# Optimization experiments

Hardware: AMD Instinct MI355X
Metric: run time of the kernel (lower is better)

Reference implementation:

```python
import jax, jax.numpy as jnp
import numpy as np

DIM = 1024
HEADS = 16
HEAD_DIM = DIM // HEADS
WINDOW = 128


def setup_inputs() -> dict:
    key = jax.random.key(0)
    k1, k2, k3, k4 = jax.random.split(key, 4)
    B, T = 2, 2048
    x = jax.random.normal(k1, (B, T, DIM), dtype=jnp.float32)
    # nn.Linear(dim, 3*dim, bias=False): weight [3*dim, dim]; y = x @ W.T
    W_qkv = jax.random.normal(k2, (3 * DIM, DIM), dtype=jnp.float32) * (1.0 / np.sqrt(DIM))
    W_proj = jax.random.normal(k3, (DIM, DIM), dtype=jnp.float32) * (1.0 / np.sqrt(DIM))
    b_proj = jax.random.normal(k4, (DIM,), dtype=jnp.float32) * 0.01
    return {"x": x, "W_qkv": W_qkv, "W_proj": W_proj, "b_proj": b_proj}


def reference(x, W_qkv, W_proj, b_proj) -> jnp.ndarray:
    B, T, C = x.shape
    scale = HEAD_DIM ** -0.5
    qkv = jnp.einsum('btc,oc->bto', x, W_qkv)  # [B,T,3*D]
    qkv = qkv.reshape(B, T, 3, HEADS, HEAD_DIM)
    qkv = jnp.transpose(qkv, (2, 0, 3, 1, 4))  # [3,B,H,T,hd]
    q, k, v = qkv[0], qkv[1], qkv[2]
    # sliding-window mask: attend iff |i-j| <= WINDOW
    idx = jnp.arange(T)
    mask = jnp.abs(idx[:, None] - idx[None, :]) <= WINDOW  # [T,T]
    scores = jnp.einsum('bhqd,bhkd->bhqk', q, k) * scale  # [B,H,T,T]
    scores = jnp.where(mask[None, None], scores, jnp.finfo(scores.dtype).min)
    attn = jax.nn.softmax(scores, axis=-1)
    out = jnp.einsum('bhqk,bhkd->bhqd', attn, v)  # [B,H,T,hd]
    out = jnp.transpose(out, (0, 2, 1, 3)).reshape(B, T, C)
    return jnp.einsum('btc,oc->bto', out, W_proj) + b_proj
```

## Files before the change

kernel.cpp:

```cpp
#include <hip/hip_runtime.h>
#include <hip/hip_bf16.h>
#include <cstdint>
#include <cstddef>

#define DIMC 1024
#define HEADS 16
#define HD 64
#define WINDOW 128
#define BB 2
#define TT 2048
#define NTOK (BB*TT)
#define QKVN (3*DIMC)

typedef __bf16 bf16;
typedef __bf16 bf16x8 __attribute__((ext_vector_type(8)));
typedef __bf16 bf16x4 __attribute__((ext_vector_type(4)));
typedef float f32x4 __attribute__((ext_vector_type(4)));
typedef unsigned int u32;

typedef const __attribute__((address_space(1))) u32* gp1_t;
typedef __attribute__((address_space(3))) u32* lp3_t;

__device__ __forceinline__ void gload16(const void* g, void* l) {
  __builtin_amdgcn_global_load_lds((gp1_t)g, (lp3_t)l, 16, 0, 0);
}

__device__ __forceinline__ u32 lds_u32(const void* p) {
  return (u32)(uintptr_t)(__attribute__((address_space(3))) const void*)p;
}

__device__ __forceinline__ void BAR() {
  asm volatile("" ::: "memory");
  __builtin_amdgcn_s_barrier();
  asm volatile("" ::: "memory");
}

__global__ void cast3_kernel(const float* __restrict__ x,
                             const float* __restrict__ wq,
                             const float* __restrict__ wp,
                             bf16* __restrict__ xo,
                             bf16* __restrict__ wqo,
                             bf16* __restrict__ wpo) {
  const int NX = NTOK * DIMC / 4;
  const int NQ = QKVN * DIMC / 4;
  const int NP = DIMC * DIMC / 4;
  const int total = NX + NQ + NP;
  typedef float float4v __attribute__((ext_vector_type(4)));
  for (int i = blockIdx.x * blockDim.x + threadIdx.x; i < total;
       i += gridDim.x * blockDim.x) {
    const float4v* src; bf16* dst; int j;
    if (i < NX)            { src = (const float4v*)x;  dst = xo;  j = i; }
    else if (i < NX + NQ)  { src = (const float4v*)wq; dst = wqo; j = i - NX; }
    else                   { src = (const float4v*)wp; dst = wpo; j = i - NX - NQ; }
    float4v v = src[j];
    bf16x4 o;
    o[0] = (bf16)v[0]; o[1] = (bf16)v[1]; o[2] = (bf16)v[2]; o[3] = (bf16)v[3];
    ((bf16x4*)dst)[j] = o;
  }
}

__device__ __forceinline__ bf16x8 lds_frag(const bf16* base, int row, int colb) {
  const char* p = (const char*)base + row * 128 + (colb ^ ((row & 7) << 4));
  return *(const bf16x8*)p;
}

template<int BN, int N_, bool BF16OUT>
__global__ __launch_bounds__(256, 2) void gemm_kernel(
    const bf16* __restrict__ A, const bf16* __restrict__ Bw,
    bf16* __restrict__ Cb, float* __restrict__ Cf,
    const float* __restrict__ bias) {
  constexpr int NT = 16;
  constexpr int NB = BN / 32;
  constexpr int LPT = 4 + BN / 32;
  __shared__ bf16 Al[2][128 * 64];
  __shared__ bf16 Bl[2][BN * 64];

  const int tid = threadIdx.x;
  const int w = tid >> 6, l = tid & 63;
  const int wm = w >> 1, wn = w & 1;
  const int lr = l & 15, lg = l >> 4;

  const int nwg = gridDim.x;
  const int bid = blockIdx.x;
  const int wg = (bid & 7) * (nwg >> 3) + (bid >> 3);
  const int bm = wg & 31;
  const int bn = wg >> 5;

  const char* Ag = (const char*)A + (size_t)(bm * 128) * 2048;
  const char* Bg = (const char*)Bw + (size_t)(bn * BN) * 2048;

  auto stageA = [&](bf16* lds, int kt) {
#pragma unroll
    for (int i = 0; i < 4; i++) {
      const int R0 = w * 32 + i * 8;
      const int r = R0 + (l >> 3);
      const char* src = Ag + (size_t)r * 2048 + kt * 128
                        + (((l & 7) * 16) ^ ((r & 7) << 4));
      gload16(src, lds + R0 * 64);
    }
  };
  auto stageB = [&](bf16* lds, int kt) {
#pragma unroll
    for (int i = 0; i < NB; i++) {
      const int R0 = w * (BN / 4) + i * 8;
      const int r = R0 + (l >> 3);
      const char* src = Bg + (size_t)r * 2048 + kt * 128
                        + (((l & 7) * 16) ^ ((r & 7) << 4));
      gload16(src, lds + R0 * 64);
    }
  };

  stageA(Al[0], 0); stageB(Bl[0], 0);
  stageA(Al[1], 1); stageB(Bl[1], 1);
  if constexpr (LPT == 7) asm volatile("s_waitcnt vmcnt(7)" ::: "memory");
  else                    asm volatile("s_waitcnt vmcnt(8)" ::: "memory");
  BAR();

  f32x4 acc[4][NB] = {};

  for (int kt = 0; kt < NT; ++kt) {
    const bf16* Ac = Al[kt & 1];
    const bf16* Bc = Bl[kt & 1];

    bf16x8 af[4][2], bf[NB][2];
#pragma unroll
    for (int m = 0; m < 4; m++)
#pragma unroll
      for (int kk = 0; kk < 2; kk++)
        af[m][kk] = lds_frag(Ac, wm * 64 + m * 16 + lr, kk * 64 + lg * 16);
#pragma unroll
    for (int n = 0; n < NB; n++)
#pragma unroll
      for (int kk = 0; kk < 2; kk++)
        bf[n][kk] = lds_frag(Bc, wn * (BN / 2) + n * 16 + lr, kk * 64 + lg * 16);

    asm volatile("s_waitcnt lgkmcnt(0)" ::: "memory");
    __builtin_amdgcn_sched_barrier(0);
    BAR();

    if (kt + 2 < NT) {
      stageA(Al[kt & 1], kt + 2);
      stageB(Bl[kt & 1], kt + 2);
    }

    __builtin_amdgcn_s_setprio(1);
#pragma unroll
    for (int kk = 0; kk < 2; kk++)
#pragma unroll
      for (int m = 0; m < 4; m++)
#pragma unroll
        for (int n = 0; n < NB; n++)
          acc[m][n] = __builtin_amdgcn_mfma_f32_16x16x32_bf16(
              af[m][kk], bf[n][kk], acc[m][n], 0, 0, 0);
    __builtin_amdgcn_s_setprio(0);

    if (kt < NT - 2) {
      if constexpr (LPT == 7) asm volatile("s_waitcnt vmcnt(7)" ::: "memory");
      else                    asm volatile("s_waitcnt vmcnt(8)" ::: "memory");
    } else {
      asm volatile("s_waitcnt vmcnt(0)" ::: "memory");
    }
    BAR();
  }

#pragma unroll
  for (int m = 0; m < 4; m++) {
    const int row = bm * 128 + wm * 64 + m * 16 + lg * 4;
#pragma unroll
    for (int n = 0; n < NB; n++) {
      const int col = bn * BN + wn * (BN / 2) + n * 16 + lr;
#pragma unroll
      for (int j = 0; j < 4; j++) {
        if constexpr (BF16OUT)
          Cb[(size_t)(row + j) * N_ + col] = (bf16)acc[m][n][j];
        else
          Cf[(size_t)(row + j) * N_ + col] = acc[m][n][j] + bias[col];
      }
    }
  }
}

__global__ __launch_bounds__(256, 2) void attn_kernel(const bf16* __restrict__ qkv,
                                                      bf16* __restrict__ out) {
  __shared__ bf16 Kl[3][64 * 64];
  __shared__ bf16 Vl[3][64 * 64];

  const int tid = threadIdx.x, w = tid >> 6, l = tid & 63;
  const int qb = blockIdx.x & 15, bh = blockIdx.x >> 4;
  const int b = bh >> 4, h = bh & 15;
  const int q0 = qb * 128;
  const int lr = l & 15, lg = l >> 4;
  const float SC = 0.18033688011f;

  const char* qkv_b = (const char*)qkv + (size_t)(b * TT) * (QKVN * 2);

  size_t koff[2]; u32 kdst[2];
#pragma unroll
  for (int i = 0; i < 2; i++) {
    const int R0 = 8 * (w + 4 * i);
    const int r = R0 + (l >> 3);
    const int colb = (((l & 7) * 16) ^ (((l >> 3) & 7) << 4));
    koff[i] = (size_t)r * (QKVN * 2) + (DIMC + h * HD) * 2 + colb;
    kdst[i] = (u32)(R0 * 64);
  }
  size_t voff[2]; u32 vdst[2];
#pragma unroll
  for (int i = 0; i < 2; i++) {
    const int c = tid + 256 * i;
    const int t = c >> 3, w_ = c & 7;
    const int kv = (t & 15) * 4 + (w_ >> 1);
    const int d  = (t >> 4) * 16 + (w_ & 1) * 8;
    voff[i] = (size_t)kv * (QKVN * 2) + (2 * DIMC + h * HD + d) * 2;
    vdst[i] = (u32)((w + 4 * i) * 512);
  }

  auto stage = [&](int buf, int kb) {
    const char* rowb = qkv_b + (size_t)(kb * 64) * (QKVN * 2);
#pragma unroll
    for (int i = 0; i < 2; i++)
      gload16(rowb + koff[i], &Kl[buf][kdst[i]]);
#pragma unroll
    for (int i = 0; i < 2; i++)
      gload16(rowb + voff[i], &Vl[buf][vdst[i]]);
  };

  bf16x8 qf[2][2];
#pragma unroll
  for (int qi = 0; qi < 2; qi++) {
    const bf16* qp = qkv + (size_t)(b * TT + q0 + w * 32 + qi * 16 + lr) * QKVN
                     + h * HD + lg * 8;
    qf[qi][0] = *(const bf16x8*)qp;
    qf[qi][1] = *(const bf16x8*)(qp + 32);
  }

  f32x4 Oa[2][4] = {};
  float mrow[2] = {-1e30f, -1e30f}, lrow[2] = {0.f, 0.f};

  int kb0 = 2 * qb - 2; if (kb0 < 0) kb0 = 0;
  int kb1 = 2 * qb + 3; if (kb1 > 31) kb1 = 31;

  stage(0, kb0);
  stage(1, kb0 + 1);
  asm volatile("s_waitcnt vmcnt(4)" ::: "memory");
  BAR();

  for (int kb = kb0; kb <= kb1; ++kb) {
    const int c = (kb - kb0) % 3;
    if (kb + 2 <= kb1) stage((c + 2) % 3, kb + 2);

    const bf16* Kb = &Kl[c][0];
    f32x4 Sa[2][4] = {};
#pragma unroll
    for (int kf = 0; kf < 2; kf++)
#pragma unroll
      for (int nf = 0; nf < 4; nf++) {
        const char* kp = (const char*)Kb + (nf * 16 + lr) * 128
                         + ((kf * 64 + lg * 16) ^ ((lr & 7) << 4));
        bf16x8 kfr = *(const bf16x8*)kp;
        Sa[0][nf] = __builtin_amdgcn_mfma_f32_16x16x32_bf16(kfr, qf[0][kf], Sa[0][nf], 0, 0, 0);
        Sa[1][nf] = __builtin_amdgcn_mfma_f32_16x16x32_bf16(kfr, qf[1][kf], Sa[1][nf], 0, 0, 0);
      }

    bf16x4 tr0[4][2], tr1[4][2];
    {
      const u32 vbase = lds_u32(&Vl[c][0]) + l * 8;
#pragma unroll
      for (int nf = 0; nf < 4; nf++)
#pragma unroll
        for (int kf = 0; kf < 2; kf++) {
          const u32 a = vbase + (u32)((nf * 16 + kf * 8) * 128);
          asm volatile("ds_read_b64_tr_b16 %0, %1"
                       : "=v"(tr0[nf][kf]) : "v"(a));
          asm volatile("ds_read_b64_tr_b16 %0, %1 offset:512"
                       : "=v"(tr1[nf][kf]) : "v"(a));
        }
    }

    const int kvb = kb * 64;
    float scl[2];
    bf16x8 pa[2][2];
#pragma unroll
    for (int qi = 0; qi < 2; qi++) {
      const int qrow = q0 + w * 32 + qi * 16 + lr;
      float mblk = -1e30f;
#pragma unroll
      for (int nf = 0; nf < 4; nf++)
#pragma unroll
        for (int j = 0; j < 4; j++) {
          int kv = kvb + nf * 16 + lg * 4 + j;
          int dq = qrow - kv;
          float s = Sa[qi][nf][j] * SC;
          if (dq > WINDOW || dq < -WINDOW) s = -1e30f;
          Sa[qi][nf][j] = s;
          mblk = fmaxf(mblk, s);
        }
      mblk = fmaxf(mblk, __shfl_xor(mblk, 16));
      mblk = fmaxf(mblk, __shfl_xor(mblk, 32));

      float mn = fmaxf(mrow[qi], mblk);
      scl[qi] = exp2f(mrow[qi] - mn);
      mrow[qi] = mn;

      float rsum = 0.f;
#pragma unroll
      for (int nf = 0; nf < 4; nf++)
#pragma unroll
        for (int j = 0; j < 4; j++) {
          float e = exp2f(Sa[qi][nf][j] - mn);
          Sa[qi][nf][j] = e;
          rsum += e;
        }
      rsum += __shfl_xor(rsum, 16);
      rsum += __shfl_xor(rsum, 32);
      lrow[qi] = lrow[qi] * scl[qi] + rsum;

#pragma unroll
      for (int kf = 0; kf < 2; kf++)
#pragma unroll
        for (int e = 0; e < 4; e++) {
          pa[qi][kf][e]     = (bf16)Sa[qi][2 * kf][e];
          pa[qi][kf][e + 4] = (bf16)Sa[qi][2 * kf + 1][e];
        }

#pragma unroll
      for (int j = 0; j < 4; j++) {
        float so = __shfl(scl[qi], lg * 4 + j);
#pragma unroll
        for (int nf = 0; nf < 4; nf++) Oa[qi][nf][j] *= so;
      }
    }

    asm volatile("s_waitcnt lgkmcnt(0)" ::: "memory");
    __builtin_amdgcn_sched_barrier(0);
#pragma unroll
    for (int nf = 0; nf < 4; nf++)
#pragma unroll
      for (int kf = 0; kf < 2; kf++) {
        bf16x8 vb;
#pragma unroll
        for (int e = 0; e < 4; e++) {
          vb[e]     = tr0[nf][kf][e];
          vb[e + 4] = tr1[nf][kf][e];
        }
        Oa[0][nf] = __builtin_amdgcn_mfma_f32_16x16x32_bf16(pa[0][kf], vb, Oa[0][nf], 0, 0, 0);
        Oa[1][nf] = __builtin_amdgcn_mfma_f32_16x16x32_bf16(pa[1][kf], vb, Oa[1][nf], 0, 0, 0);
      }

    if (kb < kb1) {
      if (kb + 2 <= kb1) asm volatile("s_waitcnt vmcnt(4)" ::: "memory");
      else               asm volatile("s_waitcnt vmcnt(0)" ::: "memory");
    }
    BAR();
  }

#pragma unroll
  for (int qi = 0; qi < 2; qi++) {
    float lo[4];
#pragma unroll
    for (int j = 0; j < 4; j++) lo[j] = __shfl(lrow[qi], lg * 4 + j);
#pragma unroll
    for (int nf = 0; nf < 4; nf++) {
#pragma unroll
      for (int j = 0; j < 4; j++) {
        int q = q0 + w * 32 + qi * 16 + lg * 4 + j;
        int d = nf * 16 + lr;
        out[(size_t)(b * TT + q) * DIMC + h * HD + d] = (bf16)(Oa[qi][nf][j] / lo[j]);
      }
    }
  }
}

extern "C" void kernel_launch(void* const* d_in, const int* in_sizes, int n_in,
                              void* d_out, int out_size, void* d_ws, size_t ws_size,
                              hipStream_t stream) {
  const float* x     = (const float*)d_in[0];
  const float* Wqkv  = (const float*)d_in[1];
  const float* Wproj = (const float*)d_in[2];
  const float* bproj = (const float*)d_in[3];
  float* out = (float*)d_out;

  char* ws = (char*)d_ws;
  bf16* xb   = (bf16*)(ws);
  bf16* wqb  = (bf16*)(ws + 8388608);
  bf16* wpb  = (bf16*)(ws + 14680064);
  bf16* qkvb = (bf16*)(ws + 16777216);
  bf16* aob  = (bf16*)(ws + 41943040);

  cast3_kernel<<<2048, 256, 0, stream>>>(x, Wqkv, Wproj, xb, wqb, wpb);
  gemm_kernel<96, QKVN, true><<<1024, 256, 0, stream>>>(xb, wqb, qkvb, nullptr, nullptr);
  attn_kernel<<<512, 256, 0, stream>>>(qkvb, aob);
  gemm_kernel<128, DIMC, false><<<256, 256, 0, stream>>>(aob, wpb, nullptr, out, bproj);
}
```

Baseline: 90.04 us.

## Retile QKV and proj GEMMs, enlarge attention blocks, add lazy softmax rescale

The QKV GEMM becomes a dedicated kernel with 128x192 tiles, where each wave owns all 128 rows and a 48-column slice, launched on 512 blocks. The projection GEMM moves to 512-thread blocks with 64-wide N tiles and a new grouped block-to-tile mapping. Attention uses 512-thread blocks covering 256 queries, so each K/V block is loaded once for more queries. The online softmax now skips rescaling O and l unless the block max exceeds the running max by more than 8 (in log2 units), which cuts exp and multiply work at the cost of a larger bounded range for the exponentials.

```diff
diff --git a/kernel.cpp b/kernel.cpp
--- a/kernel.cpp
+++ b/kernel.cpp
@@ -64,35 +64,29 @@
   return *(const bf16x8*)p;
 }
 
-template<int BN, int N_, bool BF16OUT>
-__global__ __launch_bounds__(256, 2) void gemm_kernel(
+__global__ __launch_bounds__(256, 2) void gemm_qkv_kernel(
     const bf16* __restrict__ A, const bf16* __restrict__ Bw,
-    bf16* __restrict__ Cb, float* __restrict__ Cf,
-    const float* __restrict__ bias) {
+    bf16* __restrict__ C) {
   constexpr int NT = 16;
-  constexpr int NB = BN / 32;
-  constexpr int LPT = 4 + BN / 32;
   __shared__ bf16 Al[2][128 * 64];
-  __shared__ bf16 Bl[2][BN * 64];
+  __shared__ bf16 Bl[2][192 * 64];
 
   const int tid = threadIdx.x;
   const int w = tid >> 6, l = tid & 63;
-  const int wm = w >> 1, wn = w & 1;
   const int lr = l & 15, lg = l >> 4;
 
-  const int nwg = gridDim.x;
   const int bid = blockIdx.x;
-  const int wg = (bid & 7) * (nwg >> 3) + (bid >> 3);
-  const int bm = wg & 31;
-  const int bn = wg >> 5;
+  const int x = bid & 7, i = bid >> 3;
+  const int bm = 8 * (x >> 1) + (i & 7);
+  const int bn = 8 * (x & 1) + (i >> 3);
 
   const char* Ag = (const char*)A + (size_t)(bm * 128) * 2048;
-  const char* Bg = (const char*)Bw + (size_t)(bn * BN) * 2048;
+  const char* Bg = (const char*)Bw + (size_t)(bn * 192) * 2048;
 
   auto stageA = [&](bf16* lds, int kt) {
 #pragma unroll
-    for (int i = 0; i < 4; i++) {
-      const int R0 = w * 32 + i * 8;
+    for (int i2 = 0; i2 < 4; i2++) {
+      const int R0 = w * 32 + i2 * 8;
       const int r = R0 + (l >> 3);
       const char* src = Ag + (size_t)r * 2048 + kt * 128
                         + (((l & 7) * 16) ^ ((r & 7) << 4));
@@ -101,8 +95,8 @@
   };
   auto stageB = [&](bf16* lds, int kt) {
 #pragma unroll
-    for (int i = 0; i < NB; i++) {
-      const int R0 = w * (BN / 4) + i * 8;
+    for (int i2 = 0; i2 < 6; i2++) {
+      const int R0 = w * 48 + i2 * 8;
       const int r = R0 + (l >> 3);
       const char* src = Bg + (size_t)r * 2048 + kt * 128
                         + (((l & 7) * 16) ^ ((r & 7) << 4));
@@ -112,16 +106,119 @@
 
   stageA(Al[0], 0); stageB(Bl[0], 0);
   stageA(Al[1], 1); stageB(Bl[1], 1);
-  if constexpr (LPT == 7) asm volatile("s_waitcnt vmcnt(7)" ::: "memory");
-  else                    asm volatile("s_waitcnt vmcnt(8)" ::: "memory");
+  asm volatile("s_waitcnt vmcnt(10)" ::: "memory");
   BAR();
 
-  f32x4 acc[4][NB] = {};
+  f32x4 acc[8][3] = {};
 
   for (int kt = 0; kt < NT; ++kt) {
     const bf16* Ac = Al[kt & 1];
     const bf16* Bc = Bl[kt & 1];
 
+    bf16x8 af[8][2], bf[3][2];
+#pragma unroll
+    for (int m = 0; m < 8; m++)
+#pragma unroll
+      for (int kk = 0; kk < 2; kk++)
+        af[m][kk] = lds_frag(Ac, m * 16 + lr, kk * 64 + lg * 16);
+#pragma unroll
+    for (int n = 0; n < 3; n++)
+#pragma unroll
+      for (int kk = 0; kk < 2; kk++)
+        bf[n][kk] = lds_frag(Bc, w * 48 + n * 16 + lr, kk * 64 + lg * 16);
+
+    asm volatile("s_waitcnt lgkmcnt(0)" ::: "memory");
+    __builtin_amdgcn_sched_barrier(0);
+    BAR();
+
+    if (kt + 2 < NT) {
+      stageA(Al[kt & 1], kt + 2);
+      stageB(Bl[kt & 1], kt + 2);
+    }
+
+    __builtin_amdgcn_s_setprio(1);
+#pragma unroll
+    for (int kk = 0; kk < 2; kk++)
+#pragma unroll
+      for (int m = 0; m < 8; m++)
+#pragma unroll
+        for (int n = 0; n < 3; n++)
+          acc[m][n] = __builtin_amdgcn_mfma_f32_16x16x32_bf16(
+              af[m][kk], bf[n][kk], acc[m][n], 0, 0, 0);
+    __builtin_amdgcn_s_setprio(0);
+
+    if (kt < NT - 2) asm volatile("s_waitcnt vmcnt(10)" ::: "memory");
+    else             asm volatile("s_waitcnt vmcnt(0)" ::: "memory");
+    BAR();
+  }
+
+#pragma unroll
+  for (int m = 0; m < 8; m++) {
+    const int row = bm * 128 + m * 16 + lg * 4;
+#pragma unroll
+    for (int n = 0; n < 3; n++) {
+      const int col = bn * 192 + w * 48 + n * 16 + lr;
+#pragma unroll
+      for (int j = 0; j < 4; j++)
+        C[(size_t)(row + j) * QKVN + col] = (bf16)acc[m][n][j];
+    }
+  }
+}
+
+template<int BN, int N_>
+__global__ __launch_bounds__(512, 2) void gemm_proj_kernel(
+    const bf16* __restrict__ A, const bf16* __restrict__ Bw,
+    float* __restrict__ Cf, const float* __restrict__ bias) {
+  constexpr int NT = 16;
+  constexpr int NB = BN / 64;
+  __shared__ bf16 Al[2][128 * 64];
+  __shared__ bf16 Bl[2][BN * 64];
+
+  const int tid = threadIdx.x;
+  const int w = tid >> 6, l = tid & 63;
+  const int wm = w >> 2, wn = w & 3;
+  const int lr = l & 15, lg = l >> 4;
+
+  const int bid = blockIdx.x;
+  const int x = bid & 7, i = bid >> 3;
+  const int bm = 8 * (x >> 1) + (i & 7);
+  const int bn = 8 * (x & 1) + (i >> 3);
+
+  const char* Ag = (const char*)A + (size_t)(bm * 128) * 2048;
+  const char* Bg = (const char*)Bw + (size_t)(bn * BN) * 2048;
+
+  auto stageA = [&](bf16* lds, int kt) {
+#pragma unroll
+    for (int i2 = 0; i2 < 2; i2++) {
+      const int R0 = w * 16 + i2 * 8;
+      const int r = R0 + (l >> 3);
+      const char* src = Ag + (size_t)r * 2048 + kt * 128
+                        + (((l & 7) * 16) ^ ((r & 7) << 4));
+      gload16(src, lds + R0 * 64);
+    }
+  };
+  auto stageB = [&](bf16* lds, int kt) {
+#pragma unroll
+    for (int i2 = 0; i2 < NB; i2++) {
+      const int R0 = w * (BN / 8) + i2 * 8;
+      const int r = R0 + (l >> 3);
+      const char* src = Bg + (size_t)r * 2048 + kt * 128
+                        + (((l & 7) * 16) ^ ((r & 7) << 4));
+      gload16(src, lds + R0 * 64);
+    }
+  };
+
+  stageA(Al[0], 0); stageB(Bl[0], 0);
+  stageA(Al[1], 1); stageB(Bl[1], 1);
+  asm volatile("s_waitcnt vmcnt(3)" ::: "memory");
+  BAR();
+
+  f32x4 acc[4][NB] = {};
+
+  for (int kt = 0; kt < NT; ++kt) {
+    const bf16* Ac = Al[kt & 1];
+    const bf16* Bc = Bl[kt & 1];
+
     bf16x8 af[4][2], bf[NB][2];
 #pragma unroll
     for (int m = 0; m < 4; m++)
@@ -132,7 +229,7 @@
     for (int n = 0; n < NB; n++)
 #pragma unroll
       for (int kk = 0; kk < 2; kk++)
-        bf[n][kk] = lds_frag(Bc, wn * (BN / 2) + n * 16 + lr, kk * 64 + lg * 16);
+        bf[n][kk] = lds_frag(Bc, wn * (BN / 4) + n * 16 + lr, kk * 64 + lg * 16);
 
     asm volatile("s_waitcnt lgkmcnt(0)" ::: "memory");
     __builtin_amdgcn_sched_barrier(0);
@@ -154,12 +251,8 @@
               af[m][kk], bf[n][kk], acc[m][n], 0, 0, 0);
     __builtin_amdgcn_s_setprio(0);
 
-    if (kt < NT - 2) {
-      if constexpr (LPT == 7) asm volatile("s_waitcnt vmcnt(7)" ::: "memory");
-      else                    asm volatile("s_waitcnt vmcnt(8)" ::: "memory");
-    } else {
-      asm volatile("s_waitcnt vmcnt(0)" ::: "memory");
-    }
+    if (kt < NT - 2) asm volatile("s_waitcnt vmcnt(3)" ::: "memory");
+    else             asm volatile("s_waitcnt vmcnt(0)" ::: "memory");
     BAR();
   }
 
@@ -168,60 +261,50 @@
     const int row = bm * 128 + wm * 64 + m * 16 + lg * 4;
 #pragma unroll
     for (int n = 0; n < NB; n++) {
-      const int col = bn * BN + wn * (BN / 2) + n * 16 + lr;
-#pragma unroll
-      for (int j = 0; j < 4; j++) {
-        if constexpr (BF16OUT)
-          Cb[(size_t)(row + j) * N_ + col] = (bf16)acc[m][n][j];
-        else
-          Cf[(size_t)(row + j) * N_ + col] = acc[m][n][j] + bias[col];
-      }
-    }
-  }
-}
-
-__global__ __launch_bounds__(256, 2) void attn_kernel(const bf16* __restrict__ qkv,
+      const int col = bn * BN + wn * (BN / 4) + n * 16 + lr;
+#pragma unroll
+      for (int j = 0; j < 4; j++)
+        Cf[(size_t)(row + j) * N_ + col] = acc[m][n][j] + bias[col];
+    }
+  }
+}
+
+__global__ __launch_bounds__(512, 2) void attn_kernel(const bf16* __restrict__ qkv,
                                                       bf16* __restrict__ out) {
   __shared__ bf16 Kl[3][64 * 64];
   __shared__ bf16 Vl[3][64 * 64];
 
   const int tid = threadIdx.x, w = tid >> 6, l = tid & 63;
-  const int qb = blockIdx.x & 15, bh = blockIdx.x >> 4;
+  const int qb = blockIdx.x & 7, bh = blockIdx.x >> 3;
   const int b = bh >> 4, h = bh & 15;
-  const int q0 = qb * 128;
+  const int q0 = qb * 256;
   const int lr = l & 15, lg = l >> 4;
   const float SC = 0.18033688011f;
 
   const char* qkv_b = (const char*)qkv + (size_t)(b * TT) * (QKVN * 2);
 
-  size_t koff[2]; u32 kdst[2];
-#pragma unroll
-  for (int i = 0; i < 2; i++) {
-    const int R0 = 8 * (w + 4 * i);
+  size_t koff; u32 kdst;
+  {
+    const int R0 = 8 * w;
     const int r = R0 + (l >> 3);
     const int colb = (((l & 7) * 16) ^ (((l >> 3) & 7) << 4));
-    koff[i] = (size_t)r * (QKVN * 2) + (DIMC + h * HD) * 2 + colb;
-    kdst[i] = (u32)(R0 * 64);
-  }
-  size_t voff[2]; u32 vdst[2];
-#pragma unroll
-  for (int i = 0; i < 2; i++) {
-    const int c = tid + 256 * i;
+    koff = (size_t)r * (QKVN * 2) + (DIMC + h * HD) * 2 + colb;
+    kdst = (u32)(R0 * 64);
+  }
+  size_t voff; u32 vdst;
+  {
+    const int c = tid;
     const int t = c >> 3, w_ = c & 7;
     const int kv = (t & 15) * 4 + (w_ >> 1);
     const int d  = (t >> 4) * 16 + (w_ & 1) * 8;
-    voff[i] = (size_t)kv * (QKVN * 2) + (2 * DIMC + h * HD + d) * 2;
-    vdst[i] = (u32)((w + 4 * i) * 512);
+    voff = (size_t)kv * (QKVN * 2) + (2 * DIMC + h * HD + d) * 2;
+    vdst = (u32)(w * 512);
   }
 
   auto stage = [&](int buf, int kb) {
     const char* rowb = qkv_b + (size_t)(kb * 64) * (QKVN * 2);
-#pragma unroll
-    for (int i = 0; i < 2; i++)
-      gload16(rowb + koff[i], &Kl[buf][kdst[i]]);
-#pragma unroll
-    for (int i = 0; i < 2; i++)
-      gload16(rowb + voff[i], &Vl[buf][vdst[i]]);
+    gload16(rowb + koff, &Kl[buf][kdst]);
+    gload16(rowb + voff, &Vl[buf][vdst]);
   };
 
   bf16x8 qf[2][2];
@@ -236,12 +319,12 @@
   f32x4 Oa[2][4] = {};
   float mrow[2] = {-1e30f, -1e30f}, lrow[2] = {0.f, 0.f};
 
-  int kb0 = 2 * qb - 2; if (kb0 < 0) kb0 = 0;
-  int kb1 = 2 * qb + 3; if (kb1 > 31) kb1 = 31;
+  int kb0 = 4 * qb - 2; if (kb0 < 0) kb0 = 0;
+  int kb1 = 4 * qb + 5; if (kb1 > 31) kb1 = 31;
 
   stage(0, kb0);
   stage(1, kb0 + 1);
-  asm volatile("s_waitcnt vmcnt(4)" ::: "memory");
+  asm volatile("s_waitcnt vmcnt(2)" ::: "memory");
   BAR();
 
   for (int kb = kb0; kb <= kb1; ++kb) {
@@ -277,7 +360,6 @@
     }
 
     const int kvb = kb * 64;
-    float scl[2];
     bf16x8 pa[2][2];
 #pragma unroll
     for (int qi = 0; qi < 2; qi++) {
@@ -297,22 +379,31 @@
       mblk = fmaxf(mblk, __shfl_xor(mblk, 16));
       mblk = fmaxf(mblk, __shfl_xor(mblk, 32));
 
-      float mn = fmaxf(mrow[qi], mblk);
-      scl[qi] = exp2f(mrow[qi] - mn);
-      mrow[qi] = mn;
+      if (!__all(mblk <= mrow[qi] + 8.f)) {
+        float mn = fmaxf(mrow[qi], mblk);
+        float sc = exp2f(mrow[qi] - mn);
+        mrow[qi] = mn;
+        lrow[qi] *= sc;
+#pragma unroll
+        for (int j = 0; j < 4; j++) {
+          float so = __shfl(sc, lg * 4 + j);
+#pragma unroll
+          for (int nf = 0; nf < 4; nf++) Oa[qi][nf][j] *= so;
+        }
+      }
 
       float rsum = 0.f;
 #pragma unroll
       for (int nf = 0; nf < 4; nf++)
 #pragma unroll
         for (int j = 0; j < 4; j++) {
-          float e = exp2f(Sa[qi][nf][j] - mn);
+          float e = exp2f(Sa[qi][nf][j] - mrow[qi]);
           Sa[qi][nf][j] = e;
           rsum += e;
         }
       rsum += __shfl_xor(rsum, 16);
       rsum += __shfl_xor(rsum, 32);
-      lrow[qi] = lrow[qi] * scl[qi] + rsum;
+      lrow[qi] += rsum;
 
 #pragma unroll
       for (int kf = 0; kf < 2; kf++)
@@ -321,13 +412,6 @@
           pa[qi][kf][e]     = (bf16)Sa[qi][2 * kf][e];
           pa[qi][kf][e + 4] = (bf16)Sa[qi][2 * kf + 1][e];
         }
-
-#pragma unroll
-      for (int j = 0; j < 4; j++) {
-        float so = __shfl(scl[qi], lg * 4 + j);
-#pragma unroll
-        for (int nf = 0; nf < 4; nf++) Oa[qi][nf][j] *= so;
-      }
     }
 
     asm volatile("s_waitcnt lgkmcnt(0)" ::: "memory");
@@ -347,7 +431,7 @@
       }
 
     if (kb < kb1) {
-      if (kb + 2 <= kb1) asm volatile("s_waitcnt vmcnt(4)" ::: "memory");
+      if (kb + 2 <= kb1) asm volatile("s_waitcnt vmcnt(2)" ::: "memory");
       else               asm volatile("s_waitcnt vmcnt(0)" ::: "memory");
     }
     BAR();
@@ -387,7 +471,7 @@
   bf16* aob  = (bf16*)(ws + 41943040);
 
   cast3_kernel<<<2048, 256, 0, stream>>>(x, Wqkv, Wproj, xb, wqb, wpb);
-  gemm_kernel<96, QKVN, true><<<1024, 256, 0, stream>>>(xb, wqb, qkvb, nullptr, nullptr);
-  attn_kernel<<<512, 256, 0, stream>>>(qkvb, aob);
-  gemm_kernel<128, DIMC, false><<<256, 256, 0, stream>>>(aob, wpb, nullptr, out, bproj);
-}
+  gemm_qkv_kernel<<<512, 256, 0, stream>>>(xb, wqb, qkvb);
+  attn_kernel<<<256, 512, 0, stream>>>(qkvb, aob);
+  gemm_proj_kernel<64, DIMC><<<512, 512, 0, stream>>>(aob, wpb, out, bproj);
+}
```

After: 81.71 us. -9.3%, faster.
